# Optimization experiments

Hardware: AMD Instinct MI355X
Metric: run time of the kernel (lower is better)

Reference implementation:

```python
import jax, jax.numpy as jnp
import numpy as np

N, C, H, W = 4, 256, 64, 64
K, G, PAD, STRIDE, DIL = 3, 8, 1, 1, 1
GC = C // G      # channels per group
P = K * K        # sampling points per group
HIN, WIN = H + 2 * PAD, W + 2 * PAD
BN_EPS = 1e-5
LN_EPS = 1e-5


def setup_inputs():
    key = jax.random.key(0)
    ks = jax.random.split(key, 8)
    f32 = jnp.float32
    return {
        "x": jax.random.normal(ks[0], (N, C, H, W), dtype=f32),
        "w_in": jax.random.normal(ks[1], (C, C), dtype=f32) * 0.05,
        "b_in": jnp.zeros((C,), f32),
        "w_dw": jax.random.normal(ks[2], (C, 1, K, K), dtype=f32) * 0.1,
        "b_dw": jnp.zeros((C,), f32),
        "ln_g": jnp.ones((C,), f32), "ln_b": jnp.zeros((C,), f32),
        "w_off": jax.random.normal(ks[3], (C, G * P * 2), dtype=f32) * 0.01,
        "b_off": jax.random.normal(ks[4], (G * P * 2,), dtype=f32) * 0.01,
        "w_mask": jax.random.normal(ks[5], (C, G * P), dtype=f32) * 0.01,
        "b_mask": jnp.zeros((G * P,), f32),
        "w_out": jax.random.normal(ks[6], (C, C), dtype=f32) * 0.05,
        "b_out": jnp.zeros((C,), f32),
        "bn_g": jnp.ones((C,), f32), "bn_b": jnp.zeros((C,), f32),
        "bn_mean": jnp.zeros((C,), f32), "bn_var": jnp.ones((C,), f32),
    }


def _bilinear(img, grid):
    # img: (B, Cc, Hh, Ww); grid: (B, S, P, 2) normalized to [-1,1],
    # matches F.grid_sample(mode='bilinear', padding_mode='zeros', align_corners=False)
    B, Cc, Hh, Ww = img.shape
    gx = (grid[..., 0] + 1.0) * 0.5 * Ww - 0.5
    gy = (grid[..., 1] + 1.0) * 0.5 * Hh - 0.5
    x0 = jnp.floor(gx)
    y0 = jnp.floor(gy)
    wx = gx - x0
    wy = gy - y0
    flat = img.reshape(B, Cc, Hh * Ww)

    def tap(xi, yi, wgt):
        valid = (xi >= 0) & (xi <= Ww - 1) & (yi >= 0) & (yi <= Hh - 1)
        idx = (jnp.clip(yi, 0, Hh - 1) * Ww + jnp.clip(xi, 0, Ww - 1)).astype(jnp.int32)
        v = jax.vmap(lambda im, ix: im[:, ix])(flat, idx)   # (B, Cc, S, P)
        return v * (wgt * valid.astype(img.dtype))[:, None]

    return (tap(x0, y0, (1 - wx) * (1 - wy)) + tap(x0 + 1, y0, wx * (1 - wy))
            + tap(x0, y0 + 1, (1 - wx) * wy) + tap(x0 + 1, y0 + 1, wx * wy))


def _forward(x, w_in, b_in, w_dw, b_dw, ln_g, ln_b, w_off, b_off,
             w_mask, b_mask, w_out, b_out, bn_g, bn_b, bn_mean, bn_var):
    xl = jnp.transpose(x, (0, 2, 3, 1))                      # (N,H,W,C) channels-last
    x_proj = xl @ w_in + b_in                                # input_proj
    # depthwise conv + LayerNorm + GELU feature branch for offset/mask prediction
    dw = jax.lax.conv_general_dilated(
        x, w_dw, (1, 1), ((PAD, PAD), (PAD, PAD)),
        feature_group_count=C, dimension_numbers=("NCHW", "OIHW", "NCHW"))
    dw = jnp.transpose(dw + b_dw[None, :, None, None], (0, 2, 3, 1))
    mu = dw.mean(-1, keepdims=True)
    var = ((dw - mu) ** 2).mean(-1, keepdims=True)
    dw = (dw - mu) * jax.lax.rsqrt(var + LN_EPS) * ln_g + ln_b
    x1 = jax.nn.gelu(dw, approximate=False)
    offset = x1 @ w_off + b_off                              # (N,H,W,G*P*2)
    mask = jax.nn.softmax((x1 @ w_mask + b_mask).reshape(N, H, W, G, P), axis=-1)
    # reference points + dilation kernel grid, normalized to padded input, (x,y) order
    ry = ((DIL * (K - 1)) // 2 + 0.5 + jnp.arange(H, dtype=x.dtype) * STRIDE) / HIN
    rx = ((DIL * (K - 1)) // 2 + 0.5 + jnp.arange(W, dtype=x.dtype) * STRIDE) / WIN
    ref = jnp.stack(jnp.broadcast_arrays(rx[None, :], ry[:, None]), axis=-1)  # (H,W,2)
    px = (jnp.arange(K, dtype=x.dtype) * DIL - (DIL * (K - 1)) // 2) / WIN
    py = (jnp.arange(K, dtype=x.dtype) * DIL - (DIL * (K - 1)) // 2) / HIN
    gx, gy = jnp.meshgrid(px, py, indexing="ij")             # kw-major flattening as in DCNv3
    kgrid = jnp.stack([gx, gy], -1).reshape(P, 2)
    norm = jnp.array([WIN, HIN], dtype=x.dtype)
    loc = (ref[None, :, :, None, None, :] + kgrid[None, None, None, None, :, :]
           + offset.reshape(N, H, W, G, P, 2) / norm)        # (N,H,W,G,P,2), offset_scale=1
    sgrid = 2.0 * loc - 1.0
    # group-split padded value tensor and deformable sampling
    xp = jnp.pad(x_proj, ((0, 0), (PAD, PAD), (PAD, PAD), (0, 0)))
    img = jnp.transpose(xp, (0, 3, 1, 2)).reshape(N * G, GC, HIN, WIN)
    sg = jnp.transpose(sgrid.reshape(N, H * W, G, P, 2), (0, 2, 1, 3, 4)).reshape(N * G, H * W, P, 2)
    sampled = _bilinear(img, sg)                             # (N*G, GC, H*W, P)
    m = jnp.transpose(mask.reshape(N, H * W, G, P), (0, 2, 1, 3)).reshape(N * G, 1, H * W, P)
    agg = (sampled * m).sum(-1)                              # (N*G, GC, H*W)
    y = jnp.transpose(agg.reshape(N, C, H * W), (0, 2, 1)).reshape(N, H, W, C)
    y = y @ w_out + b_out                                    # output_proj
    y = jnp.transpose(y, (0, 3, 1, 2))                       # back to NCHW
    y = (y - bn_mean[None, :, None, None]) * jax.lax.rsqrt(bn_var + BN_EPS)[None, :, None, None]
    y = y * bn_g[None, :, None, None] + bn_b[None, :, None, None]
    return y * jax.nn.sigmoid(y)                             # SiLU (Conv.default_act)


def reference(x, w_in, b_in, w_dw, b_dw, ln_g, ln_b, w_off, b_off,
              w_mask, b_mask, w_out, b_out, bn_g, bn_b, bn_mean, bn_var):
    return _forward(x, w_in, b_in, w_dw, b_dw, ln_g, ln_b, w_off, b_off,
                    w_mask, b_mask, w_out, b_out, bn_g, bn_b, bn_mean, bn_var)
```

## Files before the change

kernel.cpp:

```cpp
#include <hip/hip_runtime.h>
#include <math.h>

#define NB   4
#define CCH  256
#define HH   64
#define WW   64
#define GG   8
#define GCH  32
#define PP   9
#define HIN  66
#define WIN  66
#define HWSZ 4096
#define NPIX 16384

#define XP_ELEMS  (NB*HIN*WIN*CCH)
#define X1_ELEMS  (NPIX*CCH)
#define AGG_ELEMS (NPIX*CCH)
#define OFF_ELEMS (NPIX*144)
#define MSK_ELEMS (NPIX*72)

typedef __attribute__((ext_vector_type(8))) short bf16x8;
typedef __attribute__((ext_vector_type(4))) float f32x4;

__device__ __forceinline__ unsigned short f2bf(float f) {
    unsigned int u = __float_as_uint(f);
    unsigned int r = (u + 0x7FFFu + ((u >> 16) & 1u)) >> 16;
    return (unsigned short)r;
}
__device__ __forceinline__ float bf2f(unsigned short s) {
    return __uint_as_float(((unsigned int)s) << 16);
}
__device__ __forceinline__ unsigned int f2bf_pk(float lo, float hi) {
    return (unsigned int)f2bf(lo) | ((unsigned int)f2bf(hi) << 16);
}

#define AK 40

__global__ __launch_bounds__(64) void k_zero_ring(unsigned short* __restrict__ xp)
{
    int b = blockIdx.x;
    int n = b / 260;
    int rp = b % 260;
    int h, w;
    if (rp < 66)       { h = 0;        w = rp; }
    else if (rp < 132) { h = 65;       w = rp - 66; }
    else if (rp < 196) { h = rp - 131; w = 0; }
    else               { h = rp - 195; w = 65; }
    uint2 z = make_uint2(0u, 0u);
    *(uint2*)&xp[(((size_t)n * HIN + h) * WIN + w) * CCH + threadIdx.x * 4] = z;
}

__global__ __launch_bounds__(256) void k_gemm_in(
    const float* __restrict__ x, const float* __restrict__ w_in,
    const float* __restrict__ b_in, unsigned short* __restrict__ xp)
{
    __shared__ short As[128 * AK];
    __shared__ short Ws[64 * AK];

    const int m0  = blockIdx.x * 128;
    const int co0 = blockIdx.y * 64;
    const int tid = threadIdx.x;
    const int n   = m0 >> 12;
    const int hw0 = m0 & 4095;

    const int wave = tid >> 6;
    const int lane = tid & 63;
    const int r16  = lane & 15;
    const int quad = lane >> 4;
    const int mw   = wave * 32;

    const float* xa = x + (size_t)n * CCH * HWSZ + hw0;

    f32x4 acc[2][4];
#pragma unroll
    for (int i = 0; i < 2; i++)
#pragma unroll
        for (int j = 0; j < 4; j++) acc[i][j] = (f32x4){0.f, 0.f, 0.f, 0.f};

    float apre[16];
    float wpre[8];

#pragma unroll
    for (int l = 0; l < 8; l++) {
        int idx = tid + l * 256;
        int m = idx & 127, kp = idx >> 7;
        apre[2 * l + 0] = xa[(size_t)(2 * kp) * HWSZ + m];
        apre[2 * l + 1] = xa[(size_t)(2 * kp + 1) * HWSZ + m];
    }
#pragma unroll
    for (int l = 0; l < 4; l++) {
        int idx = tid + l * 256;
        int nn = idx & 63, kp = idx >> 6;
        wpre[2 * l + 0] = w_in[(size_t)(2 * kp) * CCH + co0 + nn];
        wpre[2 * l + 1] = w_in[(size_t)(2 * kp + 1) * CCH + co0 + nn];
    }

    for (int k0 = 0; k0 < CCH; k0 += 32) {
#pragma unroll
        for (int l = 0; l < 8; l++) {
            int idx = tid + l * 256;
            int m = idx & 127, kp = idx >> 7;
            ((unsigned int*)As)[(m * AK) / 2 + kp] = f2bf_pk(apre[2 * l], apre[2 * l + 1]);
        }
#pragma unroll
        for (int l = 0; l < 4; l++) {
            int idx = tid + l * 256;
            int nn = idx & 63, kp = idx >> 6;
            ((unsigned int*)Ws)[(nn * AK) / 2 + kp] = f2bf_pk(wpre[2 * l], wpre[2 * l + 1]);
        }
        __syncthreads();

        if (k0 + 32 < CCH) {
            int k1 = k0 + 32;
#pragma unroll
            for (int l = 0; l < 8; l++) {
                int idx = tid + l * 256;
                int m = idx & 127, kp = idx >> 7;
                apre[2 * l + 0] = xa[(size_t)(k1 + 2 * kp) * HWSZ + m];
                apre[2 * l + 1] = xa[(size_t)(k1 + 2 * kp + 1) * HWSZ + m];
            }
#pragma unroll
            for (int l = 0; l < 4; l++) {
                int idx = tid + l * 256;
                int nn = idx & 63, kp = idx >> 6;
                wpre[2 * l + 0] = w_in[(size_t)(k1 + 2 * kp) * CCH + co0 + nn];
                wpre[2 * l + 1] = w_in[(size_t)(k1 + 2 * kp + 1) * CCH + co0 + nn];
            }
        }

        bf16x8 a0 = *(const bf16x8*)&As[(mw + r16) * AK + quad * 8];
        bf16x8 a1 = *(const bf16x8*)&As[(mw + 16 + r16) * AK + quad * 8];
#pragma unroll
        for (int nt = 0; nt < 4; nt++) {
            bf16x8 bfr = *(const bf16x8*)&Ws[(nt * 16 + r16) * AK + quad * 8];
            acc[0][nt] = __builtin_amdgcn_mfma_f32_16x16x32_bf16(a0, bfr, acc[0][nt], 0, 0, 0);
            acc[1][nt] = __builtin_amdgcn_mfma_f32_16x16x32_bf16(a1, bfr, acc[1][nt], 0, 0, 0);
        }
        __syncthreads();
    }

#pragma unroll
    for (int nt = 0; nt < 4; nt++) {
        int co = co0 + nt * 16 + r16;
        float bias = b_in[co];
#pragma unroll
        for (int mt = 0; mt < 2; mt++) {
            int mbase = mw + mt * 16 + quad * 4;
#pragma unroll
            for (int r = 0; r < 4; r++) {
                int hw = hw0 + mbase + r;
                int h = hw >> 6, w = hw & 63;
                xp[(((size_t)n * HIN + (h + 1)) * WIN + (w + 1)) * CCH + co] =
                    f2bf(acc[mt][nt][r] + bias);
            }
        }
    }
}

#define SDW_STRIDE 258
__global__ __launch_bounds__(512) void k_dw_ln_gelu(
    const float* __restrict__ x, const float* __restrict__ w_dw,
    const float* __restrict__ b_dw, const float* __restrict__ ln_g,
    const float* __restrict__ ln_b, unsigned short* __restrict__ x1)
{
    __shared__ unsigned short sdw[64 * SDW_STRIDE];
    __shared__ float r1s[8][64];
    __shared__ float r2s[8][64];
    __shared__ float mu_s[64];
    __shared__ float rs_s[64];

    const int h = blockIdx.x;
    const int n = blockIdx.y;
    const int tid = threadIdx.x;
    const int wave = tid >> 6;
    const int lane = tid & 63;

    const float* xn = x + (size_t)n * CCH * HWSZ;
    const bool h0ok = (h > 0);
    const bool h2ok = (h < HH - 1);

    float s1 = 0.f, s2 = 0.f;

#pragma unroll 4
    for (int it = 0; it < 32; it++) {
        const int c = it * 8 + wave;
        const float* xc = xn + (size_t)c * HWSZ + h * WW + lane;
        float v0 = h0ok ? xc[-WW] : 0.f;
        float v1 = xc[0];
        float v2 = h2ok ? xc[WW] : 0.f;

        const float* wk = w_dw + c * 9;
        float acc = b_dw[c];

        float l0 = __shfl_up(v0, 1);  if (lane == 0)  l0 = 0.f;
        float r0 = __shfl_down(v0, 1); if (lane == 63) r0 = 0.f;
        acc += wk[0] * l0 + wk[1] * v0 + wk[2] * r0;

        float l1 = __shfl_up(v1, 1);  if (lane == 0)  l1 = 0.f;
        float r1 = __shfl_down(v1, 1); if (lane == 63) r1 = 0.f;
        acc += wk[3] * l1 + wk[4] * v1 + wk[5] * r1;

        float l2 = __shfl_up(v2, 1);  if (lane == 0)  l2 = 0.f;
        float r2 = __shfl_down(v2, 1); if (lane == 63) r2 = 0.f;
        acc += wk[6] * l2 + wk[7] * v2 + wk[8] * r2;

        s1 += acc;
        s2 += acc * acc;
        sdw[lane * SDW_STRIDE + c] = f2bf(acc);
    }

    r1s[wave][lane] = s1;
    r2s[wave][lane] = s2;
    __syncthreads();

    if (tid < 64) {
        float a1 = 0.f, a2 = 0.f;
#pragma unroll
        for (int q = 0; q < 8; q++) { a1 += r1s[q][tid]; a2 += r2s[q][tid]; }
        float mu = a1 * (1.0f / 256.0f);
        float var = a2 * (1.0f / 256.0f) - mu * mu;
        mu_s[tid] = mu;
        rs_s[tid] = rsqrtf(var + 1e-5f);
    }
    __syncthreads();

    const int c0 = (tid & 63) * 4;
    const int wq = tid >> 6;
    float g4[4], b4[4];
#pragma unroll
    for (int i = 0; i < 4; i++) { g4[i] = ln_g[c0 + i]; b4[i] = ln_b[c0 + i]; }

    unsigned short* x1p = x1 + (((size_t)n * HH + h) * WW) * CCH + c0;
#pragma unroll
    for (int pass = 0; pass < 8; pass++) {
        int w = wq + pass * 8;
        float mu = mu_s[w], rs = rs_s[w];
        const unsigned short* row = &sdw[w * SDW_STRIDE + c0];
        unsigned short tmp[4];
#pragma unroll
        for (int i = 0; i < 4; i++) {
            float v = (bf2f(row[i]) - mu) * rs * g4[i] + b4[i];
            tmp[i] = f2bf(0.5f * v * (1.0f + erff(v * 0.70710678118654752f)));
        }
        ushort4 o; o.x = tmp[0]; o.y = tmp[1]; o.z = tmp[2]; o.w = tmp[3];
        *(ushort4*)&x1p[(size_t)w * CCH] = o;
    }
}

__global__ __launch_bounds__(256) void k_gemm_offmask(
    const unsigned short* __restrict__ x1, const float* __restrict__ w_off,
    const float* __restrict__ b_off, const float* __restrict__ w_mask,
    const float* __restrict__ b_mask, float* __restrict__ off,
    float* __restrict__ msk)
{
    __shared__ short As[128 * AK];
    __shared__ short Ws[64 * AK];

    const int m0  = blockIdx.x * 128;
    const int co0 = blockIdx.y * 64;
    const int tid = threadIdx.x;

    const int wave = tid >> 6;
    const int lane = tid & 63;
    const int r16  = lane & 15;
    const int quad = lane >> 4;
    const int mw   = wave * 32;

    const int am = tid >> 2, akq = tid & 3;
    const int wn = tid & 63, wkp = tid >> 6;

    f32x4 acc[2][4];
#pragma unroll
    for (int i = 0; i < 2; i++)
#pragma unroll
        for (int j = 0; j < 4; j++) acc[i][j] = (f32x4){0.f, 0.f, 0.f, 0.f};

    uint4 apre[2];
    float wpre[8];

#pragma unroll
    for (int l = 0; l < 2; l++) {
        int m = am + l * 64;
        apre[l] = *(const uint4*)&x1[(size_t)(m0 + m) * CCH + akq * 8];
    }
#pragma unroll
    for (int l = 0; l < 4; l++) {
        int kp = wkp + l * 4;
        int col = co0 + wn;
        float v0 = 0.f, v1 = 0.f;
        if (col < 144) {
            v0 = w_off[(size_t)(2 * kp) * 144 + col];
            v1 = w_off[(size_t)(2 * kp + 1) * 144 + col];
        } else if (col < 216) {
            v0 = w_mask[(size_t)(2 * kp) * 72 + col - 144];
            v1 = w_mask[(size_t)(2 * kp + 1) * 72 + col - 144];
        }
        wpre[2 * l] = v0; wpre[2 * l + 1] = v1;
    }

    for (int k0 = 0; k0 < CCH; k0 += 32) {
#pragma unroll
        for (int l = 0; l < 2; l++) {
            int m = am + l * 64;
            *(uint4*)&As[m * AK + akq * 8] = apre[l];
        }
#pragma unroll
        for (int l = 0; l < 4; l++) {
            int kp = wkp + l * 4;
            ((unsigned int*)Ws)[(wn * AK) / 2 + kp] = f2bf_pk(wpre[2 * l], wpre[2 * l + 1]);
        }
        __syncthreads();

        if (k0 + 32 < CCH) {
            int k1 = k0 + 32;
#pragma unroll
            for (int l = 0; l < 2; l++) {
                int m = am + l * 64;
                apre[l] = *(const uint4*)&x1[(size_t)(m0 + m) * CCH + k1 + akq * 8];
            }
#pragma unroll
            for (int l = 0; l < 4; l++) {
                int kp = wkp + l * 4;
                int col = co0 + wn;
                float v0 = 0.f, v1 = 0.f;
                if (col < 144) {
                    v0 = w_off[(size_t)(k1 + 2 * kp) * 144 + col];
                    v1 = w_off[(size_t)(k1 + 2 * kp + 1) * 144 + col];
                } else if (col < 216) {
                    v0 = w_mask[(size_t)(k1 + 2 * kp) * 72 + col - 144];
                    v1 = w_mask[(size_t)(k1 + 2 * kp + 1) * 72 + col - 144];
                }
                wpre[2 * l] = v0; wpre[2 * l + 1] = v1;
            }
        }

        bf16x8 a0 = *(const bf16x8*)&As[(mw + r16) * AK + quad * 8];
        bf16x8 a1 = *(const bf16x8*)&As[(mw + 16 + r16) * AK + quad * 8];
#pragma unroll
        for (int nt = 0; nt < 4; nt++) {
            bf16x8 bfr = *(const bf16x8*)&Ws[(nt * 16 + r16) * AK + quad * 8];
            acc[0][nt] = __builtin_amdgcn_mfma_f32_16x16x32_bf16(a0, bfr, acc[0][nt], 0, 0, 0);
            acc[1][nt] = __builtin_amdgcn_mfma_f32_16x16x32_bf16(a1, bfr, acc[1][nt], 0, 0, 0);
        }
        __syncthreads();
    }

#pragma unroll
    for (int nt = 0; nt < 4; nt++) {
        int col = co0 + nt * 16 + r16;
        if (col >= 216) continue;
        float bias = (col < 144) ? b_off[col] : b_mask[col - 144];
#pragma unroll
        for (int mt = 0; mt < 2; mt++) {
            int mbase = m0 + mw + mt * 16 + quad * 4;
#pragma unroll
            for (int r = 0; r < 4; r++) {
                int p = mbase + r;
                float v = acc[mt][nt][r] + bias;
                if (col < 144) off[(size_t)p * 144 + col] = v;
                else           msk[(size_t)p * 72 + col - 144] = v;
            }
        }
    }
}

__device__ __forceinline__ void acc8_tap(float* a, uint4 vv, float wgt) {
    a[0] += wgt * __uint_as_float(vv.x << 16);
    a[1] += wgt * __uint_as_float(vv.x & 0xffff0000u);
    a[2] += wgt * __uint_as_float(vv.y << 16);
    a[3] += wgt * __uint_as_float(vv.y & 0xffff0000u);
    a[4] += wgt * __uint_as_float(vv.z << 16);
    a[5] += wgt * __uint_as_float(vv.z & 0xffff0000u);
    a[6] += wgt * __uint_as_float(vv.w << 16);
    a[7] += wgt * __uint_as_float(vv.w & 0xffff0000u);
}

__global__ __launch_bounds__(256) void k_sample_agg(
    const unsigned short* __restrict__ xp, const float* __restrict__ off,
    const float* __restrict__ msk, unsigned short* __restrict__ agg)
{
    __shared__ float  sm[576];
    __shared__ int2   tco[576];
    __shared__ float4 twt[576];

    const int tid = threadIdx.x;
    const int s0 = blockIdx.x * 8;

    if (tid < 64) {
        const int pix = tid >> 3, g = tid & 7;
        const float* mskp = msk + (size_t)(s0 + pix) * 72 + g * 9;
        float e[9];
        float mx = -1e30f;
#pragma unroll
        for (int p = 0; p < PP; p++) { e[p] = mskp[p]; mx = fmaxf(mx, e[p]); }
        float sum = 0.f;
#pragma unroll
        for (int p = 0; p < PP; p++) { e[p] = __expf(e[p] - mx); sum += e[p]; }
        float rs = 1.0f / sum;
#pragma unroll
        for (int p = 0; p < PP; p++) sm[tid * 9 + p] = e[p] * rs;
    }
    __syncthreads();

    for (int idx = tid; idx < 576; idx += 256) {
        int pix = idx / 72;
        int rem = idx - pix * 72;
        int g = rem / 9;
        int p = rem - g * 9;
        int s = s0 + pix;
        int hw = s & 4095;
        int h = hw >> 6, w = hw & 63;
        const float* offp = off + (size_t)s * 144 + g * 18 + p * 2;
        float ox = offp[0], oy = offp[1];
        int i = p / 3, j = p - i * 3;
        float fx = (float)(w + i) + ox;
        float fy = (float)(h + j) + oy;
        float x0f = floorf(fx), y0f = floorf(fy);
        int x0 = (int)x0f, y0 = (int)y0f;
        float wx = fx - x0f, wy = fy - y0f;
        float m = sm[idx];
        float w00 = (1.f - wx) * (1.f - wy) * m;
        float w10 = wx * (1.f - wy) * m;
        float w01 = (1.f - wx) * wy * m;
        float w11 = wx * wy * m;
        int x1c = x0 + 1, y1c = y0 + 1;
        if (!((x0  >= 0) && (x0  < WIN))) { w00 = 0.f; w01 = 0.f; }
        if (!((x1c >= 0) && (x1c < WIN))) { w10 = 0.f; w11 = 0.f; }
        if (!((y0  >= 0) && (y0  < HIN))) { w00 = 0.f; w10 = 0.f; }
        if (!((y1c >= 0) && (y1c < HIN))) { w01 = 0.f; w11 = 0.f; }
        int cx0 = min(max(x0, 0), WIN - 1), cx1 = min(max(x1c, 0), WIN - 1);
        int cy0 = min(max(y0, 0), HIN - 1), cy1 = min(max(y1c, 0), HIN - 1);
        tco[idx] = make_int2(cx0 | (cx1 << 16), cy0 | (cy1 << 16));
        twt[idx] = make_float4(w00, w10, w01, w11);
    }
    __syncthreads();

    const int pix = tid >> 5;
    const int l5 = tid & 31;
    const int g = l5 >> 2, c8 = l5 & 3;
    const int s = s0 + pix;
    const int n = s >> 12;
    const unsigned short* base = xp + (size_t)n * HIN * WIN * CCH + g * GCH + c8 * 8;
    const int tbase = pix * 72 + g * 9;

    float a[8];
#pragma unroll
    for (int i = 0; i < 8; i++) a[i] = 0.f;

#pragma unroll
    for (int p = 0; p < PP; p++) {
        int2 cc = tco[tbase + p];
        float4 wt = twt[tbase + p];
        int cx0 = cc.x & 0xFFFF, cx1 = cc.x >> 16;
        int cy0 = cc.y & 0xFFFF, cy1 = cc.y >> 16;
        const unsigned short* r0 = base + (size_t)(cy0 * WIN) * CCH;
        const unsigned short* r1 = base + (size_t)(cy1 * WIN) * CCH;
        uint4 v00 = *(const uint4*)&r0[(size_t)cx0 * CCH];
        uint4 v10 = *(const uint4*)&r0[(size_t)cx1 * CCH];
        uint4 v01 = *(const uint4*)&r1[(size_t)cx0 * CCH];
        uint4 v11 = *(const uint4*)&r1[(size_t)cx1 * CCH];
        acc8_tap(a, v00, wt.x);
        acc8_tap(a, v10, wt.y);
        acc8_tap(a, v01, wt.z);
        acc8_tap(a, v11, wt.w);
    }

    uint4 o;
    o.x = (unsigned int)f2bf(a[0]) | ((unsigned int)f2bf(a[1]) << 16);
    o.y = (unsigned int)f2bf(a[2]) | ((unsigned int)f2bf(a[3]) << 16);
    o.z = (unsigned int)f2bf(a[4]) | ((unsigned int)f2bf(a[5]) << 16);
    o.w = (unsigned int)f2bf(a[6]) | ((unsigned int)f2bf(a[7]) << 16);
    *(uint4*)&agg[(size_t)s * CCH + g * GCH + c8 * 8] = o;
}

__global__ __launch_bounds__(256) void k_gemm_out(
    const unsigned short* __restrict__ agg, const float* __restrict__ w_out,
    const float* __restrict__ b_out, const float* __restrict__ bn_g,
    const float* __restrict__ bn_b, const float* __restrict__ bn_mean,
    const float* __restrict__ bn_var, float* __restrict__ out)
{
    __shared__ short As[128 * AK];
    __shared__ short Ws[64 * AK];

    const int m0  = blockIdx.x * 128;
    const int co0 = blockIdx.y * 64;
    const int tid = threadIdx.x;
    const int n   = m0 >> 12;
    const int hw0 = m0 & 4095;

    const int wave = tid >> 6;
    const int lane = tid & 63;
    const int r16  = lane & 15;
    const int quad = lane >> 4;
    const int mw   = wave * 32;

    const int am = tid >> 2, akq = tid & 3;
    const int wn = tid & 63, wkp = tid >> 6;

    f32x4 acc[2][4];
#pragma unroll
    for (int i = 0; i < 2; i++)
#pragma unroll
        for (int j = 0; j < 4; j++) acc[i][j] = (f32x4){0.f, 0.f, 0.f, 0.f};

    uint4 apre[2];
    float wpre[8];

#pragma unroll
    for (int l = 0; l < 2; l++) {
        int m = am + l * 64;
        apre[l] = *(const uint4*)&agg[(size_t)(m0 + m) * CCH + akq * 8];
    }
#pragma unroll
    for (int l = 0; l < 4; l++) {
        int kp = wkp + l * 4;
        wpre[2 * l + 0] = w_out[(size_t)(2 * kp) * CCH + co0 + wn];
        wpre[2 * l + 1] = w_out[(size_t)(2 * kp + 1) * CCH + co0 + wn];
    }

    for (int k0 = 0; k0 < CCH; k0 += 32) {
#pragma unroll
        for (int l = 0; l < 2; l++) {
            int m = am + l * 64;
            *(uint4*)&As[m * AK + akq * 8] = apre[l];
        }
#pragma unroll
        for (int l = 0; l < 4; l++) {
            int kp = wkp + l * 4;
            ((unsigned int*)Ws)[(wn * AK) / 2 + kp] = f2bf_pk(wpre[2 * l], wpre[2 * l + 1]);
        }
        __syncthreads();

        if (k0 + 32 < CCH) {
            int k1 = k0 + 32;
#pragma unroll
            for (int l = 0; l < 2; l++) {
                int m = am + l * 64;
                apre[l] = *(const uint4*)&agg[(size_t)(m0 + m) * CCH + k1 + akq * 8];
            }
#pragma unroll
            for (int l = 0; l < 4; l++) {
                int kp = wkp + l * 4;
                wpre[2 * l + 0] = w_out[(size_t)(k1 + 2 * kp) * CCH + co0 + wn];
                wpre[2 * l + 1] = w_out[(size_t)(k1 + 2 * kp + 1) * CCH + co0 + wn];
            }
        }

        bf16x8 a0 = *(const bf16x8*)&As[(mw + r16) * AK + quad * 8];
        bf16x8 a1 = *(const bf16x8*)&As[(mw + 16 + r16) * AK + quad * 8];
#pragma unroll
        for (int nt = 0; nt < 4; nt++) {
            bf16x8 bfr = *(const bf16x8*)&Ws[(nt * 16 + r16) * AK + quad * 8];
            acc[0][nt] = __builtin_amdgcn_mfma_f32_16x16x32_bf16(a0, bfr, acc[0][nt], 0, 0, 0);
            acc[1][nt] = __builtin_amdgcn_mfma_f32_16x16x32_bf16(a1, bfr, acc[1][nt], 0, 0, 0);
        }
        __syncthreads();
    }

#pragma unroll
    for (int nt = 0; nt < 4; nt++) {
        int co = co0 + nt * 16 + r16;
        float mean = bn_mean[co];
        float rstd = rsqrtf(bn_var[co] + 1e-5f);
        float gg = bn_g[co], bb = bn_b[co], bo = b_out[co];
#pragma unroll
        for (int mt = 0; mt < 2; mt++) {
            int hwb = hw0 + mw + mt * 16 + quad * 4;
            float tmp[4];
#pragma unroll
            for (int r = 0; r < 4; r++) {
                float y = acc[mt][nt][r] + bo;
                float yh = (y - mean) * rstd * gg + bb;
                tmp[r] = yh / (1.0f + __expf(-yh));
            }
            float4 v = make_float4(tmp[0], tmp[1], tmp[2], tmp[3]);
            *(float4*)&out[((size_t)n * CCH + co) * HWSZ + hwb] = v;
        }
    }
}

extern "C" void kernel_launch(void* const* d_in, const int* in_sizes, int n_in,
                              void* d_out, int out_size, void* d_ws, size_t ws_size,
                              hipStream_t stream)
{
    const float* x       = (const float*)d_in[0];
    const float* w_in    = (const float*)d_in[1];
    const float* b_in    = (const float*)d_in[2];
    const float* w_dw    = (const float*)d_in[3];
    const float* b_dw    = (const float*)d_in[4];
    const float* ln_g    = (const float*)d_in[5];
    const float* ln_b    = (const float*)d_in[6];
    const float* w_off   = (const float*)d_in[7];
    const float* b_off   = (const float*)d_in[8];
    const float* w_mask  = (const float*)d_in[9];
    const float* b_mask  = (const float*)d_in[10];
    const float* w_out   = (const float*)d_in[11];
    const float* b_out   = (const float*)d_in[12];
    const float* bn_g    = (const float*)d_in[13];
    const float* bn_b    = (const float*)d_in[14];
    const float* bn_mean = (const float*)d_in[15];
    const float* bn_var  = (const float*)d_in[16];
    float* out = (float*)d_out;

    unsigned short* xp  = (unsigned short*)d_ws;
    unsigned short* x1  = xp + XP_ELEMS;
    unsigned short* agg = x1 + X1_ELEMS;
    float* off = (float*)(agg + AGG_ELEMS);
    float* msk = off + OFF_ELEMS;

    k_zero_ring<<<dim3(1040), 64, 0, stream>>>(xp);
    k_gemm_in<<<dim3(128, 4), 256, 0, stream>>>(x, w_in, b_in, xp);
    k_dw_ln_gelu<<<dim3(64, 4), 512, 0, stream>>>(x, w_dw, b_dw, ln_g, ln_b, x1);
    k_gemm_offmask<<<dim3(128, 4), 256, 0, stream>>>(x1, w_off, b_off, w_mask, b_mask, off, msk);
    k_sample_agg<<<dim3(2048), 256, 0, stream>>>(xp, off, msk, agg);
    k_gemm_out<<<dim3(128, 4), 256, 0, stream>>>(agg, w_out, b_out, bn_g, bn_b, bn_mean, bn_var, out);
}
```

Measured before the change: 181.4 us.

## Merge front kernels into one launch and double-buffer GEMM shared tiles

The ring-zeroing, input-projection GEMM and depthwise+LayerNorm+GELU kernels become one kernel that dispatches on block index, so the independent stages run side by side in a single launch. The depthwise branch moves from 512 to 256 threads per block. All three MFMA GEMMs now double-buffer their LDS tiles, which drops one barrier per k-step and lets the next tile's global loads overlap the current MFMAs. The cost is more LDS per block, which may lower occupancy, plus branch divergence across block roles in the merged kernel.

```diff
diff --git a/kernel.cpp b/kernel.cpp
--- a/kernel.cpp
+++ b/kernel.cpp
@@ -35,215 +35,211 @@
 }
 
 #define AK 40
-
-__global__ __launch_bounds__(64) void k_zero_ring(unsigned short* __restrict__ xp)
+#define SDW_STRIDE 258
+
+__global__ __launch_bounds__(256) void k_front(
+    const float* __restrict__ x, const float* __restrict__ w_in,
+    const float* __restrict__ b_in, const float* __restrict__ w_dw,
+    const float* __restrict__ b_dw, const float* __restrict__ ln_g,
+    const float* __restrict__ ln_b, unsigned short* __restrict__ xp,
+    unsigned short* __restrict__ x1)
 {
-    int b = blockIdx.x;
-    int n = b / 260;
-    int rp = b % 260;
-    int h, w;
-    if (rp < 66)       { h = 0;        w = rp; }
-    else if (rp < 132) { h = 65;       w = rp - 66; }
-    else if (rp < 196) { h = rp - 131; w = 0; }
-    else               { h = rp - 195; w = 65; }
-    uint2 z = make_uint2(0u, 0u);
-    *(uint2*)&xp[(((size_t)n * HIN + h) * WIN + w) * CCH + threadIdx.x * 4] = z;
-}
-
-__global__ __launch_bounds__(256) void k_gemm_in(
-    const float* __restrict__ x, const float* __restrict__ w_in,
-    const float* __restrict__ b_in, unsigned short* __restrict__ xp)
-{
-    __shared__ short As[128 * AK];
-    __shared__ short Ws[64 * AK];
-
-    const int m0  = blockIdx.x * 128;
-    const int co0 = blockIdx.y * 64;
+    __shared__ __align__(16) char smem[35584];
+    const int b = blockIdx.x;
     const int tid = threadIdx.x;
-    const int n   = m0 >> 12;
-    const int hw0 = m0 & 4095;
-
-    const int wave = tid >> 6;
-    const int lane = tid & 63;
-    const int r16  = lane & 15;
-    const int quad = lane >> 4;
-    const int mw   = wave * 32;
-
-    const float* xa = x + (size_t)n * CCH * HWSZ + hw0;
-
-    f32x4 acc[2][4];
-#pragma unroll
-    for (int i = 0; i < 2; i++)
-#pragma unroll
-        for (int j = 0; j < 4; j++) acc[i][j] = (f32x4){0.f, 0.f, 0.f, 0.f};
-
-    float apre[16];
-    float wpre[8];
-
-#pragma unroll
-    for (int l = 0; l < 8; l++) {
-        int idx = tid + l * 256;
-        int m = idx & 127, kp = idx >> 7;
-        apre[2 * l + 0] = xa[(size_t)(2 * kp) * HWSZ + m];
-        apre[2 * l + 1] = xa[(size_t)(2 * kp + 1) * HWSZ + m];
-    }
-#pragma unroll
-    for (int l = 0; l < 4; l++) {
-        int idx = tid + l * 256;
-        int nn = idx & 63, kp = idx >> 6;
-        wpre[2 * l + 0] = w_in[(size_t)(2 * kp) * CCH + co0 + nn];
-        wpre[2 * l + 1] = w_in[(size_t)(2 * kp + 1) * CCH + co0 + nn];
-    }
-
-    for (int k0 = 0; k0 < CCH; k0 += 32) {
-#pragma unroll
-        for (int l = 0; l < 8; l++) {
-            int idx = tid + l * 256;
-            int m = idx & 127, kp = idx >> 7;
-            ((unsigned int*)As)[(m * AK) / 2 + kp] = f2bf_pk(apre[2 * l], apre[2 * l + 1]);
-        }
-#pragma unroll
-        for (int l = 0; l < 4; l++) {
-            int idx = tid + l * 256;
-            int nn = idx & 63, kp = idx >> 6;
-            ((unsigned int*)Ws)[(nn * AK) / 2 + kp] = f2bf_pk(wpre[2 * l], wpre[2 * l + 1]);
-        }
-        __syncthreads();
-
-        if (k0 + 32 < CCH) {
-            int k1 = k0 + 32;
+
+    if (b < 512) {
+        short* AsB = (short*)smem;
+        short* WsB = (short*)(smem + 2 * 128 * AK * sizeof(short));
+
+        const int m0  = (b & 127) * 128;
+        const int co0 = (b >> 7) * 64;
+        const int n   = m0 >> 12;
+        const int hw0 = m0 & 4095;
+
+        const int wave = tid >> 6;
+        const int lane = tid & 63;
+        const int r16  = lane & 15;
+        const int quad = lane >> 4;
+        const int mw   = wave * 32;
+
+        const float* xa = x + (size_t)n * CCH * HWSZ + hw0;
+
+        f32x4 acc[2][4];
+#pragma unroll
+        for (int i = 0; i < 2; i++)
+#pragma unroll
+            for (int j = 0; j < 4; j++) acc[i][j] = (f32x4){0.f, 0.f, 0.f, 0.f};
+
+        float apre[16], wpre[8];
+
+        auto loadT = [&](int k0) {
 #pragma unroll
             for (int l = 0; l < 8; l++) {
                 int idx = tid + l * 256;
                 int m = idx & 127, kp = idx >> 7;
-                apre[2 * l + 0] = xa[(size_t)(k1 + 2 * kp) * HWSZ + m];
-                apre[2 * l + 1] = xa[(size_t)(k1 + 2 * kp + 1) * HWSZ + m];
+                apre[2 * l + 0] = xa[(size_t)(k0 + 2 * kp) * HWSZ + m];
+                apre[2 * l + 1] = xa[(size_t)(k0 + 2 * kp + 1) * HWSZ + m];
             }
 #pragma unroll
             for (int l = 0; l < 4; l++) {
                 int idx = tid + l * 256;
                 int nn = idx & 63, kp = idx >> 6;
-                wpre[2 * l + 0] = w_in[(size_t)(k1 + 2 * kp) * CCH + co0 + nn];
-                wpre[2 * l + 1] = w_in[(size_t)(k1 + 2 * kp + 1) * CCH + co0 + nn];
-            }
-        }
-
-        bf16x8 a0 = *(const bf16x8*)&As[(mw + r16) * AK + quad * 8];
-        bf16x8 a1 = *(const bf16x8*)&As[(mw + 16 + r16) * AK + quad * 8];
+                wpre[2 * l + 0] = w_in[(size_t)(k0 + 2 * kp) * CCH + co0 + nn];
+                wpre[2 * l + 1] = w_in[(size_t)(k0 + 2 * kp + 1) * CCH + co0 + nn];
+            }
+        };
+        auto storeT = [&](int buf) {
+            short* A = AsB + buf * 128 * AK;
+            short* W = WsB + buf * 64 * AK;
+#pragma unroll
+            for (int l = 0; l < 8; l++) {
+                int idx = tid + l * 256;
+                int m = idx & 127, kp = idx >> 7;
+                ((unsigned int*)A)[(m * AK) / 2 + kp] = f2bf_pk(apre[2 * l], apre[2 * l + 1]);
+            }
+#pragma unroll
+            for (int l = 0; l < 4; l++) {
+                int idx = tid + l * 256;
+                int nn = idx & 63, kp = idx >> 6;
+                ((unsigned int*)W)[(nn * AK) / 2 + kp] = f2bf_pk(wpre[2 * l], wpre[2 * l + 1]);
+            }
+        };
+
+        loadT(0);
+        storeT(0);
+        __syncthreads();
+
+#pragma unroll
+        for (int it = 0; it < 8; it++) {
+            int cur = it & 1;
+            if (it < 7) loadT((it + 1) * 32);
+            const short* A = AsB + cur * 128 * AK;
+            const short* W = WsB + cur * 64 * AK;
+            bf16x8 a0 = *(const bf16x8*)&A[(mw + r16) * AK + quad * 8];
+            bf16x8 a1 = *(const bf16x8*)&A[(mw + 16 + r16) * AK + quad * 8];
+#pragma unroll
+            for (int nt = 0; nt < 4; nt++) {
+                bf16x8 bfr = *(const bf16x8*)&W[(nt * 16 + r16) * AK + quad * 8];
+                acc[0][nt] = __builtin_amdgcn_mfma_f32_16x16x32_bf16(a0, bfr, acc[0][nt], 0, 0, 0);
+                acc[1][nt] = __builtin_amdgcn_mfma_f32_16x16x32_bf16(a1, bfr, acc[1][nt], 0, 0, 0);
+            }
+            if (it < 7) {
+                storeT(cur ^ 1);
+                __syncthreads();
+            }
+        }
+
 #pragma unroll
         for (int nt = 0; nt < 4; nt++) {
-            bf16x8 bfr = *(const bf16x8*)&Ws[(nt * 16 + r16) * AK + quad * 8];
-            acc[0][nt] = __builtin_amdgcn_mfma_f32_16x16x32_bf16(a0, bfr, acc[0][nt], 0, 0, 0);
-            acc[1][nt] = __builtin_amdgcn_mfma_f32_16x16x32_bf16(a1, bfr, acc[1][nt], 0, 0, 0);
-        }
+            int co = co0 + nt * 16 + r16;
+            float bias = b_in[co];
+#pragma unroll
+            for (int mt = 0; mt < 2; mt++) {
+                int mbase = mw + mt * 16 + quad * 4;
+#pragma unroll
+                for (int r = 0; r < 4; r++) {
+                    int hw = hw0 + mbase + r;
+                    int h = hw >> 6, w = hw & 63;
+                    xp[(((size_t)n * HIN + (h + 1)) * WIN + (w + 1)) * CCH + co] =
+                        f2bf(acc[mt][nt][r] + bias);
+                }
+            }
+        }
+    } else if (b < 768) {
+        unsigned short* sdw = (unsigned short*)smem;
+        float* r1s = (float*)(smem + 33024);
+        float* r2s = (float*)(smem + 34048);
+        float* mu_s = (float*)(smem + 35072);
+        float* rs_s = (float*)(smem + 35328);
+
+        const int idx = b - 512;
+        const int h = idx & 63;
+        const int n = idx >> 6;
+        const int wave = tid >> 6;
+        const int lane = tid & 63;
+
+        const float* xn = x + (size_t)n * CCH * HWSZ;
+        const bool h0ok = (h > 0);
+        const bool h2ok = (h < HH - 1);
+
+        float s1 = 0.f, s2 = 0.f;
+
+#pragma unroll 4
+        for (int it = 0; it < 64; it++) {
+            const int c = it * 4 + wave;
+            const float* xc = xn + (size_t)c * HWSZ + h * WW + lane;
+            float v0 = h0ok ? xc[-WW] : 0.f;
+            float v1 = xc[0];
+            float v2 = h2ok ? xc[WW] : 0.f;
+
+            const float* wk = w_dw + c * 9;
+            float acc = b_dw[c];
+
+            float l0 = __shfl_up(v0, 1);   if (lane == 0)  l0 = 0.f;
+            float r0 = __shfl_down(v0, 1); if (lane == 63) r0 = 0.f;
+            acc += wk[0] * l0 + wk[1] * v0 + wk[2] * r0;
+
+            float l1 = __shfl_up(v1, 1);   if (lane == 0)  l1 = 0.f;
+            float r1 = __shfl_down(v1, 1); if (lane == 63) r1 = 0.f;
+            acc += wk[3] * l1 + wk[4] * v1 + wk[5] * r1;
+
+            float l2 = __shfl_up(v2, 1);   if (lane == 0)  l2 = 0.f;
+            float r2 = __shfl_down(v2, 1); if (lane == 63) r2 = 0.f;
+            acc += wk[6] * l2 + wk[7] * v2 + wk[8] * r2;
+
+            s1 += acc;
+            s2 += acc * acc;
+            sdw[lane * SDW_STRIDE + c] = f2bf(acc);
+        }
+
+        r1s[wave * 64 + lane] = s1;
+        r2s[wave * 64 + lane] = s2;
         __syncthreads();
-    }
-
-#pragma unroll
-    for (int nt = 0; nt < 4; nt++) {
-        int co = co0 + nt * 16 + r16;
-        float bias = b_in[co];
-#pragma unroll
-        for (int mt = 0; mt < 2; mt++) {
-            int mbase = mw + mt * 16 + quad * 4;
-#pragma unroll
-            for (int r = 0; r < 4; r++) {
-                int hw = hw0 + mbase + r;
-                int h = hw >> 6, w = hw & 63;
-                xp[(((size_t)n * HIN + (h + 1)) * WIN + (w + 1)) * CCH + co] =
-                    f2bf(acc[mt][nt][r] + bias);
-            }
-        }
-    }
-}
-
-#define SDW_STRIDE 258
-__global__ __launch_bounds__(512) void k_dw_ln_gelu(
-    const float* __restrict__ x, const float* __restrict__ w_dw,
-    const float* __restrict__ b_dw, const float* __restrict__ ln_g,
-    const float* __restrict__ ln_b, unsigned short* __restrict__ x1)
-{
-    __shared__ unsigned short sdw[64 * SDW_STRIDE];
-    __shared__ float r1s[8][64];
-    __shared__ float r2s[8][64];
-    __shared__ float mu_s[64];
-    __shared__ float rs_s[64];
-
-    const int h = blockIdx.x;
-    const int n = blockIdx.y;
-    const int tid = threadIdx.x;
-    const int wave = tid >> 6;
-    const int lane = tid & 63;
-
-    const float* xn = x + (size_t)n * CCH * HWSZ;
-    const bool h0ok = (h > 0);
-    const bool h2ok = (h < HH - 1);
-
-    float s1 = 0.f, s2 = 0.f;
-
-#pragma unroll 4
-    for (int it = 0; it < 32; it++) {
-        const int c = it * 8 + wave;
-        const float* xc = xn + (size_t)c * HWSZ + h * WW + lane;
-        float v0 = h0ok ? xc[-WW] : 0.f;
-        float v1 = xc[0];
-        float v2 = h2ok ? xc[WW] : 0.f;
-
-        const float* wk = w_dw + c * 9;
-        float acc = b_dw[c];
-
-        float l0 = __shfl_up(v0, 1);  if (lane == 0)  l0 = 0.f;
-        float r0 = __shfl_down(v0, 1); if (lane == 63) r0 = 0.f;
-        acc += wk[0] * l0 + wk[1] * v0 + wk[2] * r0;
-
-        float l1 = __shfl_up(v1, 1);  if (lane == 0)  l1 = 0.f;
-        float r1 = __shfl_down(v1, 1); if (lane == 63) r1 = 0.f;
-        acc += wk[3] * l1 + wk[4] * v1 + wk[5] * r1;
-
-        float l2 = __shfl_up(v2, 1);  if (lane == 0)  l2 = 0.f;
-        float r2 = __shfl_down(v2, 1); if (lane == 63) r2 = 0.f;
-        acc += wk[6] * l2 + wk[7] * v2 + wk[8] * r2;
-
-        s1 += acc;
-        s2 += acc * acc;
-        sdw[lane * SDW_STRIDE + c] = f2bf(acc);
-    }
-
-    r1s[wave][lane] = s1;
-    r2s[wave][lane] = s2;
-    __syncthreads();
-
-    if (tid < 64) {
-        float a1 = 0.f, a2 = 0.f;
-#pragma unroll
-        for (int q = 0; q < 8; q++) { a1 += r1s[q][tid]; a2 += r2s[q][tid]; }
-        float mu = a1 * (1.0f / 256.0f);
-        float var = a2 * (1.0f / 256.0f) - mu * mu;
-        mu_s[tid] = mu;
-        rs_s[tid] = rsqrtf(var + 1e-5f);
-    }
-    __syncthreads();
-
-    const int c0 = (tid & 63) * 4;
-    const int wq = tid >> 6;
-    float g4[4], b4[4];
-#pragma unroll
-    for (int i = 0; i < 4; i++) { g4[i] = ln_g[c0 + i]; b4[i] = ln_b[c0 + i]; }
-
-    unsigned short* x1p = x1 + (((size_t)n * HH + h) * WW) * CCH + c0;
-#pragma unroll
-    for (int pass = 0; pass < 8; pass++) {
-        int w = wq + pass * 8;
-        float mu = mu_s[w], rs = rs_s[w];
-        const unsigned short* row = &sdw[w * SDW_STRIDE + c0];
-        unsigned short tmp[4];
-#pragma unroll
-        for (int i = 0; i < 4; i++) {
-            float v = (bf2f(row[i]) - mu) * rs * g4[i] + b4[i];
-            tmp[i] = f2bf(0.5f * v * (1.0f + erff(v * 0.70710678118654752f)));
-        }
-        ushort4 o; o.x = tmp[0]; o.y = tmp[1]; o.z = tmp[2]; o.w = tmp[3];
-        *(ushort4*)&x1p[(size_t)w * CCH] = o;
+
+        if (tid < 64) {
+            float a1 = 0.f, a2 = 0.f;
+#pragma unroll
+            for (int q = 0; q < 4; q++) { a1 += r1s[q * 64 + tid]; a2 += r2s[q * 64 + tid]; }
+            float mu = a1 * (1.0f / 256.0f);
+            float var = a2 * (1.0f / 256.0f) - mu * mu;
+            mu_s[tid] = mu;
+            rs_s[tid] = rsqrtf(var + 1e-5f);
+        }
+        __syncthreads();
+
+        const int c0 = (tid & 63) * 4;
+        const int wq = tid >> 6;
+        float g4[4], b4[4];
+#pragma unroll
+        for (int i = 0; i < 4; i++) { g4[i] = ln_g[c0 + i]; b4[i] = ln_b[c0 + i]; }
+
+        unsigned short* x1p = x1 + (((size_t)n * HH + h) * WW) * CCH + c0;
+#pragma unroll
+        for (int pass = 0; pass < 16; pass++) {
+            int w = wq + pass * 4;
+            float mu = mu_s[w], rs = rs_s[w];
+            const unsigned short* row = &sdw[w * SDW_STRIDE + c0];
+            unsigned short tmp[4];
+#pragma unroll
+            for (int i = 0; i < 4; i++) {
+                float v = (bf2f(row[i]) - mu) * rs * g4[i] + b4[i];
+                tmp[i] = f2bf(0.5f * v * (1.0f + erff(v * 0.70710678118654752f)));
+            }
+            ushort4 o; o.x = tmp[0]; o.y = tmp[1]; o.z = tmp[2]; o.w = tmp[3];
+            *(ushort4*)&x1p[(size_t)w * CCH] = o;
+        }
+    } else {
+        int gi = (b - 768) * 256 + tid;
+        int seg = gi >> 6, ln = gi & 63;
+        int n = seg / 260, rp = seg % 260;
+        int h, w;
+        if (rp < 66)       { h = 0;        w = rp; }
+        else if (rp < 132) { h = 65;       w = rp - 66; }
+        else if (rp < 196) { h = rp - 131; w = 0; }
+        else               { h = rp - 195; w = 65; }
+        uint2 z = make_uint2(0u, 0u);
+        *(uint2*)&xp[(((size_t)n * HIN + h) * WIN + w) * CCH + ln * 4] = z;
     }
 }
 
@@ -253,8 +249,8 @@
     const float* __restrict__ b_mask, float* __restrict__ off,
     float* __restrict__ msk)
 {
-    __shared__ short As[128 * AK];
-    __shared__ short Ws[64 * AK];
+    __shared__ short As[2 * 128 * AK];
+    __shared__ short Ws[2 * 64 * AK];
 
     const int m0  = blockIdx.x * 128;
     const int co0 = blockIdx.y * 64;
@@ -278,71 +274,64 @@
     uint4 apre[2];
     float wpre[8];
 
-#pragma unroll
-    for (int l = 0; l < 2; l++) {
-        int m = am + l * 64;
-        apre[l] = *(const uint4*)&x1[(size_t)(m0 + m) * CCH + akq * 8];
-    }
-#pragma unroll
-    for (int l = 0; l < 4; l++) {
-        int kp = wkp + l * 4;
-        int col = co0 + wn;
-        float v0 = 0.f, v1 = 0.f;
-        if (col < 144) {
-            v0 = w_off[(size_t)(2 * kp) * 144 + col];
-            v1 = w_off[(size_t)(2 * kp + 1) * 144 + col];
-        } else if (col < 216) {
-            v0 = w_mask[(size_t)(2 * kp) * 72 + col - 144];
-            v1 = w_mask[(size_t)(2 * kp + 1) * 72 + col - 144];
-        }
-        wpre[2 * l] = v0; wpre[2 * l + 1] = v1;
-    }
-
-    for (int k0 = 0; k0 < CCH; k0 += 32) {
+    auto loadT = [&](int k0) {
 #pragma unroll
         for (int l = 0; l < 2; l++) {
             int m = am + l * 64;
-            *(uint4*)&As[m * AK + akq * 8] = apre[l];
+            apre[l] = *(const uint4*)&x1[(size_t)(m0 + m) * CCH + k0 + akq * 8];
         }
 #pragma unroll
         for (int l = 0; l < 4; l++) {
             int kp = wkp + l * 4;
-            ((unsigned int*)Ws)[(wn * AK) / 2 + kp] = f2bf_pk(wpre[2 * l], wpre[2 * l + 1]);
-        }
-        __syncthreads();
-
-        if (k0 + 32 < CCH) {
-            int k1 = k0 + 32;
-#pragma unroll
-            for (int l = 0; l < 2; l++) {
-                int m = am + l * 64;
-                apre[l] = *(const uint4*)&x1[(size_t)(m0 + m) * CCH + k1 + akq * 8];
-            }
-#pragma unroll
-            for (int l = 0; l < 4; l++) {
-                int kp = wkp + l * 4;
-                int col = co0 + wn;
-                float v0 = 0.f, v1 = 0.f;
-                if (col < 144) {
-                    v0 = w_off[(size_t)(k1 + 2 * kp) * 144 + col];
-                    v1 = w_off[(size_t)(k1 + 2 * kp + 1) * 144 + col];
-                } else if (col < 216) {
-                    v0 = w_mask[(size_t)(k1 + 2 * kp) * 72 + col - 144];
-                    v1 = w_mask[(size_t)(k1 + 2 * kp + 1) * 72 + col - 144];
-                }
-                wpre[2 * l] = v0; wpre[2 * l + 1] = v1;
-            }
-        }
-
-        bf16x8 a0 = *(const bf16x8*)&As[(mw + r16) * AK + quad * 8];
-        bf16x8 a1 = *(const bf16x8*)&As[(mw + 16 + r16) * AK + quad * 8];
+            int col = co0 + wn;
+            float v0 = 0.f, v1 = 0.f;
+            if (col < 144) {
+                v0 = w_off[(size_t)(k0 + 2 * kp) * 144 + col];
+                v1 = w_off[(size_t)(k0 + 2 * kp + 1) * 144 + col];
+            } else if (col < 216) {
+                v0 = w_mask[(size_t)(k0 + 2 * kp) * 72 + col - 144];
+                v1 = w_mask[(size_t)(k0 + 2 * kp + 1) * 72 + col - 144];
+            }
+            wpre[2 * l] = v0; wpre[2 * l + 1] = v1;
+        }
+    };
+    auto storeT = [&](int buf) {
+        short* A = As + buf * 128 * AK;
+        short* W = Ws + buf * 64 * AK;
+#pragma unroll
+        for (int l = 0; l < 2; l++) {
+            int m = am + l * 64;
+            *(uint4*)&A[m * AK + akq * 8] = apre[l];
+        }
+#pragma unroll
+        for (int l = 0; l < 4; l++) {
+            int kp = wkp + l * 4;
+            ((unsigned int*)W)[(wn * AK) / 2 + kp] = f2bf_pk(wpre[2 * l], wpre[2 * l + 1]);
+        }
+    };
+
+    loadT(0);
+    storeT(0);
+    __syncthreads();
+
+#pragma unroll
+    for (int it = 0; it < 8; it++) {
+        int cur = it & 1;
+        if (it < 7) loadT((it + 1) * 32);
+        const short* A = As + cur * 128 * AK;
+        const short* W = Ws + cur * 64 * AK;
+        bf16x8 a0 = *(const bf16x8*)&A[(mw + r16) * AK + quad * 8];
+        bf16x8 a1 = *(const bf16x8*)&A[(mw + 16 + r16) * AK + quad * 8];
 #pragma unroll
         for (int nt = 0; nt < 4; nt++) {
-            bf16x8 bfr = *(const bf16x8*)&Ws[(nt * 16 + r16) * AK + quad * 8];
+            bf16x8 bfr = *(const bf16x8*)&W[(nt * 16 + r16) * AK + quad * 8];
             acc[0][nt] = __builtin_amdgcn_mfma_f32_16x16x32_bf16(a0, bfr, acc[0][nt], 0, 0, 0);
             acc[1][nt] = __builtin_amdgcn_mfma_f32_16x16x32_bf16(a1, bfr, acc[1][nt], 0, 0, 0);
         }
-        __syncthreads();
+        if (it < 7) {
+            storeT(cur ^ 1);
+            __syncthreads();
+        }
     }
 
 #pragma unroll
@@ -479,8 +468,8 @@
     const float* __restrict__ bn_b, const float* __restrict__ bn_mean,
     const float* __restrict__ bn_var, float* __restrict__ out)
 {
-    __shared__ short As[128 * AK];
-    __shared__ short Ws[64 * AK];
+    __shared__ short As[2 * 128 * AK];
+    __shared__ short Ws[2 * 64 * AK];
 
     const int m0  = blockIdx.x * 128;
     const int co0 = blockIdx.y * 64;
@@ -506,55 +495,56 @@
     uint4 apre[2];
     float wpre[8];
 
-#pragma unroll
-    for (int l = 0; l < 2; l++) {
-        int m = am + l * 64;
-        apre[l] = *(const uint4*)&agg[(size_t)(m0 + m) * CCH + akq * 8];
-    }
-#pragma unroll
-    for (int l = 0; l < 4; l++) {
-        int kp = wkp + l * 4;
-        wpre[2 * l + 0] = w_out[(size_t)(2 * kp) * CCH + co0 + wn];
-        wpre[2 * l + 1] = w_out[(size_t)(2 * kp + 1) * CCH + co0 + wn];
-    }
-
-    for (int k0 = 0; k0 < CCH; k0 += 32) {
+    auto loadT = [&](int k0) {
 #pragma unroll
         for (int l = 0; l < 2; l++) {
             int m = am + l * 64;
-            *(uint4*)&As[m * AK + akq * 8] = apre[l];
+            apre[l] = *(const uint4*)&agg[(size_t)(m0 + m) * CCH + k0 + akq * 8];
         }
 #pragma unroll
         for (int l = 0; l < 4; l++) {
             int kp = wkp + l * 4;
-            ((unsigned int*)Ws)[(wn * AK) / 2 + kp] = f2bf_pk(wpre[2 * l], wpre[2 * l + 1]);
-        }
-        __syncthreads();
-
-        if (k0 + 32 < CCH) {
-            int k1 = k0 + 32;
-#pragma unroll
-            for (int l = 0; l < 2; l++) {
-                int m = am + l * 64;
-                apre[l] = *(const uint4*)&agg[(size_t)(m0 + m) * CCH + k1 + akq * 8];
-            }
-#pragma unroll
-            for (int l = 0; l < 4; l++) {
-                int kp = wkp + l * 4;
-                wpre[2 * l + 0] = w_out[(size_t)(k1 + 2 * kp) * CCH + co0 + wn];
-                wpre[2 * l + 1] = w_out[(size_t)(k1 + 2 * kp + 1) * CCH + co0 + wn];
-            }
-        }
-
-        bf16x8 a0 = *(const bf16x8*)&As[(mw + r16) * AK + quad * 8];
-        bf16x8 a1 = *(const bf16x8*)&As[(mw + 16 + r16) * AK + quad * 8];
+            wpre[2 * l + 0] = w_out[(size_t)(k0 + 2 * kp) * CCH + co0 + wn];
+            wpre[2 * l + 1] = w_out[(size_t)(k0 + 2 * kp + 1) * CCH + co0 + wn];
+        }
+    };
+    auto storeT = [&](int buf) {
+        short* A = As + buf * 128 * AK;
+        short* W = Ws + buf * 64 * AK;
+#pragma unroll
+        for (int l = 0; l < 2; l++) {
+            int m = am + l * 64;
+            *(uint4*)&A[m * AK + akq * 8] = apre[l];
+        }
+#pragma unroll
+        for (int l = 0; l < 4; l++) {
+            int kp = wkp + l * 4;
+            ((unsigned int*)W)[(wn * AK) / 2 + kp] = f2bf_pk(wpre[2 * l], wpre[2 * l + 1]);
+        }
+    };
+
+    loadT(0);
+    storeT(0);
+    __syncthreads();
+
+#pragma unroll
+    for (int it = 0; it < 8; it++) {
+        int cur = it & 1;
+        if (it < 7) loadT((it + 1) * 32);
+        const short* A = As + cur * 128 * AK;
+        const short* W = Ws + cur * 64 * AK;
+        bf16x8 a0 = *(const bf16x8*)&A[(mw + r16) * AK + quad * 8];
+        bf16x8 a1 = *(const bf16x8*)&A[(mw + 16 + r16) * AK + quad * 8];
 #pragma unroll
         for (int nt = 0; nt < 4; nt++) {
-            bf16x8 bfr = *(const bf16x8*)&Ws[(nt * 16 + r16) * AK + quad * 8];
+            bf16x8 bfr = *(const bf16x8*)&W[(nt * 16 + r16) * AK + quad * 8];
             acc[0][nt] = __builtin_amdgcn_mfma_f32_16x16x32_bf16(a0, bfr, acc[0][nt], 0, 0, 0);
             acc[1][nt] = __builtin_amdgcn_mfma_f32_16x16x32_bf16(a1, bfr, acc[1][nt], 0, 0, 0);
         }
-        __syncthreads();
+        if (it < 7) {
+            storeT(cur ^ 1);
+            __syncthreads();
+        }
     }
 
 #pragma unroll
@@ -608,9 +598,7 @@
     float* off = (float*)(agg + AGG_ELEMS);
     float* msk = off + OFF_ELEMS;
 
-    k_zero_ring<<<dim3(1040), 64, 0, stream>>>(xp);
-    k_gemm_in<<<dim3(128, 4), 256, 0, stream>>>(x, w_in, b_in, xp);
-    k_dw_ln_gelu<<<dim3(64, 4), 512, 0, stream>>>(x, w_dw, b_dw, ln_g, ln_b, x1);
+    k_front<<<dim3(1028), 256, 0, stream>>>(x, w_in, b_in, w_dw, b_dw, ln_g, ln_b, xp, x1);
     k_gemm_offmask<<<dim3(128, 4), 256, 0, stream>>>(x1, w_off, b_off, w_mask, b_mask, off, msk);
     k_sample_agg<<<dim3(2048), 256, 0, stream>>>(xp, off, msk, agg);
     k_gemm_out<<<dim3(128, 4), 256, 0, stream>>>(agg, w_out, b_out, bn_g, bn_b, bn_mean, bn_var, out);
```

New measurement: 192.4 us. 1.06x slower.
